# Performance work log

Measured on AMD Instinct MI355X. Metric: run time of the kernel, lower is better.

The kernel has to match this reference:

```python
import jax, jax.numpy as jnp
import numpy as np

B, S, D, H = 16384, 5, 512, 8
HD = D // H


def setup_inputs() -> dict:
    key = jax.random.key(0)
    ks = jax.random.split(key, 6)
    scale = 1.0 / np.sqrt(D)
    x = jax.random.normal(ks[0], (B, S, D), dtype=jnp.float32)
    Wq = jax.random.normal(ks[1], (D, D), dtype=jnp.float32) * scale
    Wk = jax.random.normal(ks[2], (D, D), dtype=jnp.float32) * scale
    Wv = jax.random.normal(ks[3], (D, D), dtype=jnp.float32) * scale
    Wo = jax.random.normal(ks[4], (D, D), dtype=jnp.float32) * scale
    bq = jnp.zeros((D,), jnp.float32)
    bk = jnp.zeros((D,), jnp.float32)
    bv = jnp.zeros((D,), jnp.float32)
    bo = jnp.zeros((D,), jnp.float32)
    # bias_init = zeros(H,5,5); bias_init[0,:,-1] = 1.0
    prop_bias = jnp.zeros((H, S, S), jnp.float32).at[0, :, -1].set(1.0)
    return {"x": x, "Wq": Wq, "bq": bq, "Wk": Wk, "bk": bk,
            "Wv": Wv, "bv": bv, "Wo": Wo, "bo": bo, "prop_bias": prop_bias}


def reference(x, Wq, bq, Wk, bk, Wv, bv, Wo, bo, prop_bias):
    b, s, d = x.shape
    # projections (torch Linear with weight stored as [in, out] here)
    q = (x @ Wq + bq).reshape(b, s, H, HD).transpose(0, 2, 1, 3)  # [b,h,s,hd]
    k = (x @ Wk + bk).reshape(b, s, H, HD).transpose(0, 2, 1, 3)
    v = (x @ Wv + bv).reshape(b, s, H, HD).transpose(0, 2, 1, 3)
    scores = jnp.einsum('bhsd,bhtd->bhst', q, k) / jnp.sqrt(jnp.float32(HD))
    scores = scores + prop_bias[None]  # learned per-head additive bias
    attn = jax.nn.softmax(scores, axis=-1)  # dropout is identity at eval
    out = jnp.einsum('bhst,bhtd->bhsd', attn, v)
    out = out.transpose(0, 2, 1, 3).reshape(b, s, d)
    return out @ Wo + bo
```

## Files before the change

kernel.cpp:

```cpp
#include <hip/hip_runtime.h>

typedef __attribute__((ext_vector_type(4))) float f32x4;
typedef __attribute__((ext_vector_type(8))) short bf16x8;
typedef __attribute__((ext_vector_type(8))) unsigned short u16x8;

__device__ __forceinline__ unsigned short f2bf(float f) {
  unsigned int u = __float_as_uint(f);
  u += 0x7FFFu + ((u >> 16) & 1u);
  return (unsigned short)(u >> 16);
}
__device__ __forceinline__ float bf2f(unsigned short s) {
  return __uint_as_float(((unsigned int)s) << 16);
}

__device__ __forceinline__ void gll16(const void* g, void* l) {
  __builtin_amdgcn_global_load_lds((const __attribute__((address_space(1))) void*)g,
                                   (__attribute__((address_space(3))) void*)l, 16, 0, 0);
}

__global__ __launch_bounds__(256) void cvt_f32_bf16(const float* __restrict__ in,
                                                    unsigned short* __restrict__ out,
                                                    int n8) {
  int i = blockIdx.x * blockDim.x + threadIdx.x;
  int stride = gridDim.x * blockDim.x;
  for (; i < n8; i += stride) {
    const float4* p = (const float4*)in + (size_t)i * 2;
    float4 a = p[0], b = p[1];
    u16x8 r;
    r[0] = f2bf(a.x); r[1] = f2bf(a.y); r[2] = f2bf(a.z); r[3] = f2bf(a.w);
    r[4] = f2bf(b.x); r[5] = f2bf(b.y); r[6] = f2bf(b.z); r[7] = f2bf(b.w);
    *(u16x8*)(out + (size_t)i * 8) = r;
  }
}

__global__ __launch_bounds__(1024) void wtrans(const float* __restrict__ W,
                                               unsigned short* __restrict__ Wt) {
  __shared__ float t[32][33];
  const int k0 = blockIdx.x * 32, n0 = blockIdx.y * 32;
  t[threadIdx.y][threadIdx.x] = W[(size_t)(k0 + threadIdx.y) * 512 + n0 + threadIdx.x];
  __syncthreads();
  Wt[(size_t)(n0 + threadIdx.y) * 512 + k0 + threadIdx.x] = f2bf(t[threadIdx.x][threadIdx.y]);
}

__global__ __launch_bounds__(256) void bcat_k(const float* __restrict__ bq,
                                              const float* __restrict__ bk,
                                              const float* __restrict__ bv,
                                              float* __restrict__ bc) {
  int i = blockIdx.x * 256 + threadIdx.x;
  if (i < 1536) {
    float v = (i < 512) ? bq[i] : (i < 1024 ? bk[i - 512] : bv[i - 1024]);
    bc[i] = v;
  }
}

template <typename OutT>
__global__ __launch_bounds__(256, 2) void gemm2p(const unsigned short* __restrict__ A,
                                                 const unsigned short* __restrict__ Bt,
                                                 const float* __restrict__ bias,
                                                 OutT* __restrict__ C,
                                                 int Ntl, int Ncols) {
  __shared__ unsigned short As[2][128 * 64];
  __shared__ unsigned short Bs[2][128 * 64];

  const int tid = threadIdx.x;
  const int lane = tid & 63;
  const int wid = tid >> 6;
  const int wr = wid >> 1, wc = wid & 1;
  const int u = lane & 15, g = lane >> 4;

  const int chunk = gridDim.x >> 3;
  const int flat = blockIdx.x;
  const int tile = (flat & 7) * chunk + (flat >> 3);
  const int mt = tile / Ntl, nt = tile - mt * Ntl;
  const int m0 = mt * 128, n0 = nt * 128;

  const unsigned short* ap[4];
  const unsigned short* bp[4];
  int ldsoff[4];
#pragma unroll
  for (int o = 0; o < 4; ++o) {
    int c = o * 256 + tid;
    int r = c >> 3, s = (c & 7) ^ (r & 7);
    ldsoff[o] = c * 8;
    ap[o] = A + (size_t)(m0 + r) * 512 + s * 8;
    bp[o] = Bt + (size_t)(n0 + r) * 512 + s * 8;
  }

  f32x4 acc[4][4] = {};

  auto STAGE = [&](int buf, int kb) {
#pragma unroll
    for (int o = 0; o < 4; ++o) gll16(ap[o] + kb, &As[buf][ldsoff[o]]);
#pragma unroll
    for (int o = 0; o < 4; ++o) gll16(bp[o] + kb, &Bs[buf][ldsoff[o]]);
  };
  auto COMPUTE = [&](int buf) {
#pragma unroll
    for (int kk = 0; kk < 2; ++kk) {
      bf16x8 af[4], bfr[4];
#pragma unroll
      for (int mf = 0; mf < 4; ++mf) {
        int r = wr * 64 + mf * 16 + u;
        int slot = (kk * 4 + g) ^ (r & 7);
        af[mf] = *(const bf16x8*)(&As[buf][r * 64 + slot * 8]);
      }
#pragma unroll
      for (int nf = 0; nf < 4; ++nf) {
        int r = wc * 64 + nf * 16 + u;
        int slot = (kk * 4 + g) ^ (r & 7);
        bfr[nf] = *(const bf16x8*)(&Bs[buf][r * 64 + slot * 8]);
      }
#pragma unroll
      for (int mf = 0; mf < 4; ++mf)
#pragma unroll
        for (int nf = 0; nf < 4; ++nf)
          acc[mf][nf] = __builtin_amdgcn_mfma_f32_16x16x32_bf16(af[mf], bfr[nf], acc[mf][nf], 0, 0, 0);
    }
  };

  STAGE(0, 0);
  __syncthreads();
#pragma unroll
  for (int kt = 0; kt < 7; ++kt) {
    STAGE((kt + 1) & 1, (kt + 1) * 64);
    COMPUTE(kt & 1);
    __syncthreads();
  }
  COMPUTE(1);

#pragma unroll
  for (int nf = 0; nf < 4; ++nf) {
    const int col = n0 + wc * 64 + nf * 16 + u;
    const float bv = bias[col];
#pragma unroll
    for (int mf = 0; mf < 4; ++mf) {
      const int rbase = m0 + wr * 64 + mf * 16 + 4 * g;
#pragma unroll
      for (int j = 0; j < 4; ++j) {
        float v = acc[mf][nf][j] + bv;
        if constexpr (sizeof(OutT) == 2) {
          ((unsigned short*)C)[(size_t)(rbase + j) * Ncols + col] = f2bf(v);
        } else {
          ((float*)C)[(size_t)(rbase + j) * Ncols + col] = v;
        }
      }
    }
  }
}

__global__ __launch_bounds__(256) void attn_s5(const unsigned short* __restrict__ qkv,
                                               const float* __restrict__ pbias,
                                               unsigned short* __restrict__ ao) {
  __shared__ float sb[200];
  if (threadIdx.x < 200) sb[threadIdx.x] = pbias[threadIdx.x];
  __syncthreads();

  const int lane = threadIdx.x & 63;
  const int p = lane >> 4, u = lane & 15;
  const int wv = blockIdx.x * (blockDim.x >> 6) + (threadIdx.x >> 6);
  const int nwv = gridDim.x * (blockDim.x >> 6);
  const int NPG = (16384 * 8) / 4;

  for (int pg = wv; pg < NPG; pg += nwv) {
    const int idx = pg * 4 + p;
    const int b = idx >> 3, h = idx & 7;
    const size_t rbase = (size_t)(b * 5) * 1536 + h * 64 + u * 4;

    float qf[5][4], kf[5][4], vf[5][4];
#pragma unroll
    for (int s = 0; s < 5; ++s) {
      ushort4 tq = *(const ushort4*)(qkv + rbase + (size_t)s * 1536);
      ushort4 tk = *(const ushort4*)(qkv + rbase + (size_t)s * 1536 + 512);
      ushort4 tv = *(const ushort4*)(qkv + rbase + (size_t)s * 1536 + 1024);
      qf[s][0] = bf2f(tq.x); qf[s][1] = bf2f(tq.y); qf[s][2] = bf2f(tq.z); qf[s][3] = bf2f(tq.w);
      kf[s][0] = bf2f(tk.x); kf[s][1] = bf2f(tk.y); kf[s][2] = bf2f(tk.z); kf[s][3] = bf2f(tk.w);
      vf[s][0] = bf2f(tv.x); vf[s][1] = bf2f(tv.y); vf[s][2] = bf2f(tv.z); vf[s][3] = bf2f(tv.w);
    }

    float sc[5][5];
#pragma unroll
    for (int s = 0; s < 5; ++s)
#pragma unroll
      for (int t = 0; t < 5; ++t)
        sc[s][t] = qf[s][0] * kf[t][0] + qf[s][1] * kf[t][1] + qf[s][2] * kf[t][2] + qf[s][3] * kf[t][3];

#pragma unroll
    for (int m = 1; m < 16; m <<= 1)
#pragma unroll
      for (int s = 0; s < 5; ++s)
#pragma unroll
        for (int t = 0; t < 5; ++t)
          sc[s][t] += __shfl_xor(sc[s][t], m, 64);

    const float* bh = &sb[h * 25];
#pragma unroll
    for (int s = 0; s < 5; ++s) {
      float r0 = sc[s][0] * 0.125f + bh[s * 5 + 0];
      float r1 = sc[s][1] * 0.125f + bh[s * 5 + 1];
      float r2 = sc[s][2] * 0.125f + bh[s * 5 + 2];
      float r3 = sc[s][3] * 0.125f + bh[s * 5 + 3];
      float r4 = sc[s][4] * 0.125f + bh[s * 5 + 4];
      float mx = fmaxf(fmaxf(fmaxf(r0, r1), fmaxf(r2, r3)), r4);
      float e0 = __expf(r0 - mx), e1 = __expf(r1 - mx), e2 = __expf(r2 - mx),
            e3 = __expf(r3 - mx), e4 = __expf(r4 - mx);
      float rd = 1.0f / (e0 + e1 + e2 + e3 + e4);
      float o0 = (e0 * vf[0][0] + e1 * vf[1][0] + e2 * vf[2][0] + e3 * vf[3][0] + e4 * vf[4][0]) * rd;
      float o1 = (e0 * vf[0][1] + e1 * vf[1][1] + e2 * vf[2][1] + e3 * vf[3][1] + e4 * vf[4][1]) * rd;
      float o2 = (e0 * vf[0][2] + e1 * vf[1][2] + e2 * vf[2][2] + e3 * vf[3][2] + e4 * vf[4][2]) * rd;
      float o3 = (e0 * vf[0][3] + e1 * vf[1][3] + e2 * vf[2][3] + e3 * vf[3][3] + e4 * vf[4][3]) * rd;
      ushort4 o;
      o.x = f2bf(o0); o.y = f2bf(o1); o.z = f2bf(o2); o.w = f2bf(o3);
      *(ushort4*)(ao + (size_t)(b * 5 + s) * 512 + h * 64 + u * 4) = o;
    }
  }
}

extern "C" void kernel_launch(void* const* d_in, const int* in_sizes, int n_in,
                              void* d_out, int out_size, void* d_ws, size_t ws_size,
                              hipStream_t stream) {
  const float* x  = (const float*)d_in[0];
  const float* Wq = (const float*)d_in[1];
  const float* bq = (const float*)d_in[2];
  const float* Wk = (const float*)d_in[3];
  const float* bk = (const float*)d_in[4];
  const float* Wv = (const float*)d_in[5];
  const float* bv = (const float*)d_in[6];
  const float* Wo = (const float*)d_in[7];
  const float* bo = (const float*)d_in[8];
  const float* pb = (const float*)d_in[9];

  char* ws = (char*)d_ws;
  unsigned short* wt_all = (unsigned short*)ws;
  unsigned short* wtO    = (unsigned short*)(ws + 1572864);
  float*          bc     = (float*)(ws + 2097152);
  unsigned short* xb     = (unsigned short*)(ws + 2103296);
  unsigned short* qkv    = (unsigned short*)(ws + 85989376);

  cvt_f32_bf16<<<2048, 256, 0, stream>>>(x, xb, 5242880);

  dim3 tb(32, 32), tg(16, 16);
  wtrans<<<tg, tb, 0, stream>>>(Wq, wt_all + 0 * 262144);
  wtrans<<<tg, tb, 0, stream>>>(Wk, wt_all + 1 * 262144);
  wtrans<<<tg, tb, 0, stream>>>(Wv, wt_all + 2 * 262144);
  wtrans<<<tg, tb, 0, stream>>>(Wo, wtO);
  bcat_k<<<6, 256, 0, stream>>>(bq, bk, bv, bc);

  gemm2p<unsigned short><<<7680, 256, 0, stream>>>(xb, wt_all, bc, qkv, 12, 1536);

  attn_s5<<<2048, 256, 0, stream>>>(qkv, pb, xb);

  gemm2p<float><<<2560, 256, 0, stream>>>(xb, wtO, bo, (float*)d_out, 4, 512);
}
```

Measured before the change: 646.1 us.

## Replace 128x128 GEMM with 256x256 8-wave pipelined GEMM kernel

Doubles the GEMM tile to 256x256 with 512 threads (8 waves in a 2x4 layout). The K loop is split into four quarter-phases that interleave async global-to-LDS loads with LDS reads and MFMA, using explicit vmcnt/lgkmcnt waits, raw barriers and s_setprio around the MFMA blocks. The aim is more data reuse per LDS byte and better overlap of memory with compute. In exchange it uses more LDS (128KB per block) and registers, which may limit occupancy, and the hand-written wait counts are fragile.

Measured after the change: 621.3 us. -3.8%, faster.

```diff
diff --git a/kernel.cpp b/kernel.cpp
--- a/kernel.cpp
+++ b/kernel.cpp
@@ -53,88 +53,128 @@
   }
 }
 
+
+#define BAR() __builtin_amdgcn_s_barrier()
+#define LGKM0() do { asm volatile("s_waitcnt lgkmcnt(0)" ::: "memory"); \
+                     __builtin_amdgcn_sched_barrier(0); } while (0)
+#define VMC(n) asm volatile("s_waitcnt vmcnt(" #n ")" ::: "memory")
+
+#define STG_A(buf, kb, ch) gll16(aBase + (size_t)(ch) * 64 * 512 + (kb), &As[buf][(ch) * 4096 + dstoff])
+#define STG_B(buf, kb, ch) gll16(bBase + (size_t)(ch) * 64 * 512 + (kb), &Bs[buf][(ch) * 4096 + dstoff])
+
+#define RD_A(buf, mh)                                                         \
+  {                                                                           \
+    _Pragma("unroll") for (int i = 0; i < 4; ++i) {                           \
+      const int r_ = (((mh) * 4 + i) * 2 + wm) * 16 + u;                      \
+      af[i][0] = *(const bf16x8*)&As[buf][r_ * 64 + aslot0];                  \
+      af[i][1] = *(const bf16x8*)&As[buf][r_ * 64 + aslot1];                  \
+    }                                                                         \
+  }
+#define RD_B(buf, nh)                                                         \
+  {                                                                           \
+    _Pragma("unroll") for (int j = 0; j < 2; ++j) {                           \
+      const int r_ = (((nh) * 2 + j) * 4 + wn) * 16 + u;                      \
+      bfr[j][0] = *(const bf16x8*)&Bs[buf][r_ * 64 + aslot0];                 \
+      bfr[j][1] = *(const bf16x8*)&Bs[buf][r_ * 64 + aslot1];                 \
+    }                                                                         \
+  }
+#define MM(mh, nh)                                                            \
+  {                                                                           \
+    _Pragma("unroll") for (int i = 0; i < 4; ++i)                             \
+      _Pragma("unroll") for (int j = 0; j < 2; ++j)                           \
+        _Pragma("unroll") for (int kk = 0; kk < 2; ++kk)                      \
+          acc[(mh) * 4 + i][(nh) * 2 + j] = __builtin_amdgcn_mfma_f32_16x16x32_bf16( \
+              af[i][kk], bfr[j][kk], acc[(mh) * 4 + i][(nh) * 2 + j], 0, 0, 0); \
+  }
+
 template <typename OutT>
-__global__ __launch_bounds__(256, 2) void gemm2p(const unsigned short* __restrict__ A,
+__global__ __launch_bounds__(512, 2) void gemm8p(const unsigned short* __restrict__ A,
                                                  const unsigned short* __restrict__ Bt,
                                                  const float* __restrict__ bias,
                                                  OutT* __restrict__ C,
                                                  int Ntl, int Ncols) {
-  __shared__ unsigned short As[2][128 * 64];
-  __shared__ unsigned short Bs[2][128 * 64];
+  __shared__ unsigned short As[2][256 * 64];
+  __shared__ unsigned short Bs[2][256 * 64];
 
   const int tid = threadIdx.x;
   const int lane = tid & 63;
   const int wid = tid >> 6;
-  const int wr = wid >> 1, wc = wid & 1;
+  const int wm = wid >> 2;
+  const int wn = wid & 3;
   const int u = lane & 15, g = lane >> 4;
 
-  const int chunk = gridDim.x >> 3;
-  const int flat = blockIdx.x;
-  const int tile = (flat & 7) * chunk + (flat >> 3);
+  const int chunkg = gridDim.x >> 3;
+  const int tile = (blockIdx.x & 7) * chunkg + (blockIdx.x >> 3);
   const int mt = tile / Ntl, nt = tile - mt * Ntl;
-  const int m0 = mt * 128, n0 = nt * 128;
-
-  const unsigned short* ap[4];
-  const unsigned short* bp[4];
-  int ldsoff[4];
-#pragma unroll
-  for (int o = 0; o < 4; ++o) {
-    int c = o * 256 + tid;
-    int r = c >> 3, s = (c & 7) ^ (r & 7);
-    ldsoff[o] = c * 8;
-    ap[o] = A + (size_t)(m0 + r) * 512 + s * 8;
-    bp[o] = Bt + (size_t)(n0 + r) * 512 + s * 8;
-  }
-
-  f32x4 acc[4][4] = {};
-
-  auto STAGE = [&](int buf, int kb) {
-#pragma unroll
-    for (int o = 0; o < 4; ++o) gll16(ap[o] + kb, &As[buf][ldsoff[o]]);
-#pragma unroll
-    for (int o = 0; o < 4; ++o) gll16(bp[o] + kb, &Bs[buf][ldsoff[o]]);
-  };
-  auto COMPUTE = [&](int buf) {
-#pragma unroll
-    for (int kk = 0; kk < 2; ++kk) {
-      bf16x8 af[4], bfr[4];
-#pragma unroll
-      for (int mf = 0; mf < 4; ++mf) {
-        int r = wr * 64 + mf * 16 + u;
-        int slot = (kk * 4 + g) ^ (r & 7);
-        af[mf] = *(const bf16x8*)(&As[buf][r * 64 + slot * 8]);
-      }
-#pragma unroll
-      for (int nf = 0; nf < 4; ++nf) {
-        int r = wc * 64 + nf * 16 + u;
-        int slot = (kk * 4 + g) ^ (r & 7);
-        bfr[nf] = *(const bf16x8*)(&Bs[buf][r * 64 + slot * 8]);
-      }
-#pragma unroll
-      for (int mf = 0; mf < 4; ++mf)
-#pragma unroll
-        for (int nf = 0; nf < 4; ++nf)
-          acc[mf][nf] = __builtin_amdgcn_mfma_f32_16x16x32_bf16(af[mf], bfr[nf], acc[mf][nf], 0, 0, 0);
-    }
-  };
-
-  STAGE(0, 0);
-  __syncthreads();
-#pragma unroll
+  const int m0 = mt * 256, n0 = nt * 256;
+
+  const int srow = tid >> 3;
+  const int sswz = ((tid & 7) ^ (srow & 7)) * 8;
+  const unsigned short* aBase = A + (size_t)(m0 + srow) * 512 + sswz;
+  const unsigned short* bBase = Bt + (size_t)(n0 + srow) * 512 + sswz;
+  const int dstoff = tid * 8;
+
+  const int aslot0 = ((0 + g) ^ (u & 7)) * 8;
+  const int aslot1 = ((4 + g) ^ (u & 7)) * 8;
+
+  f32x4 acc[8][4] = {};
+  bf16x8 af[4][2], bfr[2][2];
+
+  STG_A(0, 0, 0); STG_A(0, 0, 1); STG_B(0, 0, 0); STG_B(0, 0, 1);
+  STG_A(0, 0, 2); STG_A(0, 0, 3); STG_B(0, 0, 2); STG_B(0, 0, 3);
+  VMC(4);
+  BAR();
+
   for (int kt = 0; kt < 7; ++kt) {
-    STAGE((kt + 1) & 1, (kt + 1) * 64);
-    COMPUTE(kt & 1);
-    __syncthreads();
-  }
-  COMPUTE(1);
+    const int cb = kt & 1, nb = cb ^ 1;
+    const int kb = (kt + 1) * 64;
+    RD_A(cb, 0); RD_B(cb, 0);
+    STG_A(nb, kb, 0); STG_A(nb, kb, 1);
+    BAR(); LGKM0();
+    __builtin_amdgcn_s_setprio(1); MM(0, 0); __builtin_amdgcn_s_setprio(0);
+    VMC(2);
+    BAR();
+    RD_B(cb, 1);
+    STG_B(nb, kb, 0); STG_B(nb, kb, 1);
+    BAR(); LGKM0();
+    __builtin_amdgcn_s_setprio(1); MM(0, 1); __builtin_amdgcn_s_setprio(0);
+    BAR();
+    RD_A(cb, 1); RD_B(cb, 0);
+    STG_A(nb, kb, 2); STG_A(nb, kb, 3);
+    BAR(); LGKM0();
+    __builtin_amdgcn_s_setprio(1); MM(1, 0); __builtin_amdgcn_s_setprio(0);
+    BAR();
+    RD_B(cb, 1);
+    STG_B(nb, kb, 2); STG_B(nb, kb, 3);
+    BAR(); LGKM0();
+    __builtin_amdgcn_s_setprio(1); MM(1, 1); __builtin_amdgcn_s_setprio(0);
+    VMC(4);
+    BAR();
+  }
+
+  RD_A(1, 0); RD_B(1, 0);
+  BAR(); LGKM0();
+  __builtin_amdgcn_s_setprio(1); MM(0, 0); __builtin_amdgcn_s_setprio(0);
+  VMC(0); BAR();
+  RD_B(1, 1);
+  BAR(); LGKM0();
+  __builtin_amdgcn_s_setprio(1); MM(0, 1); __builtin_amdgcn_s_setprio(0);
+  BAR();
+  RD_A(1, 1); RD_B(1, 0);
+  BAR(); LGKM0();
+  __builtin_amdgcn_s_setprio(1); MM(1, 0); __builtin_amdgcn_s_setprio(0);
+  BAR();
+  RD_B(1, 1);
+  LGKM0();
+  __builtin_amdgcn_s_setprio(1); MM(1, 1); __builtin_amdgcn_s_setprio(0);
 
 #pragma unroll
   for (int nf = 0; nf < 4; ++nf) {
-    const int col = n0 + wc * 64 + nf * 16 + u;
+    const int col = n0 + (nf * 4 + wn) * 16 + u;
     const float bv = bias[col];
 #pragma unroll
-    for (int mf = 0; mf < 4; ++mf) {
-      const int rbase = m0 + wr * 64 + mf * 16 + 4 * g;
+    for (int mf = 0; mf < 8; ++mf) {
+      const int rbase = m0 + (mf * 2 + wm) * 16 + 4 * g;
 #pragma unroll
       for (int j = 0; j < 4; ++j) {
         float v = acc[mf][nf][j] + bv;
@@ -245,9 +285,9 @@
   wtrans<<<tg, tb, 0, stream>>>(Wo, wtO);
   bcat_k<<<6, 256, 0, stream>>>(bq, bk, bv, bc);
 
-  gemm2p<unsigned short><<<7680, 256, 0, stream>>>(xb, wt_all, bc, qkv, 12, 1536);
+  gemm8p<unsigned short><<<1920, 512, 0, stream>>>(xb, wt_all, bc, qkv, 6, 1536);
 
   attn_s5<<<2048, 256, 0, stream>>>(qkv, pb, xb);
 
-  gemm2p<float><<<2560, 256, 0, stream>>>(xb, wtO, bo, (float*)d_out, 4, 512);
-}
+  gemm8p<float><<<640, 512, 0, stream>>>(xb, wtO, bo, (float*)d_out, 2, 512);
+}
```
